# Kernel optimization log

Hardware: AMD Instinct MI355X
Metric: run time of the kernel (lower is better)

The kernel has to match this reference:

```python
import jax, jax.numpy as jnp
from jax import lax
import numpy as np

HEADS = 8
SR = 4  # sr_ratio
LN_EPS = 1e-5


def gaussian_filt(x, kernel_size, sigma):
    # depthwise gaussian blur, x: [B, C, H, W]
    ch = x.shape[1]
    c = jnp.arange(kernel_size, dtype=x.dtype)
    xx = jnp.broadcast_to(c[None, :], (kernel_size, kernel_size))
    yy = xx.T
    mean = (kernel_size - 1) / 2.0
    g = jnp.exp(-((xx - mean) ** 2 + (yy - mean) ** 2) / (2.0 * sigma * sigma))
    g = g / g.sum()  # normalization cancels the 1/(2*pi*var) factor
    kern = jnp.broadcast_to(g[None, None], (ch, 1, kernel_size, kernel_size)).astype(x.dtype)
    p = (kernel_size - 1) // 2
    return lax.conv_general_dilated(
        x, kern, (1, 1), [(p, p), (p, p)],
        dimension_numbers=('NCHW', 'OIHW', 'NCHW'), feature_group_count=ch)


def reconstruct_feature(feature, mask, kernel_size, sigma):
    if kernel_size <= 1:
        return feature
    feature = feature * mask
    out = gaussian_filt(jnp.concatenate([feature, mask], axis=1), kernel_size, sigma)
    f_int = out[:, :-1]
    m_int = out[:, -1:]
    f_int = f_int / (m_int + 1e-6)
    m_bin = (m_int > 0).astype(feature.dtype)
    f_int = f_int * m_bin
    return feature + (1.0 - mask) * f_int


def token2map(x, loc, H, W, kernel_size, sigma):
    # x: [B, N, C], loc: [B, N, 2] in [0,1]
    B, N, C = x.shape
    loc = jnp.clip(loc, 0.0, 1.0) * jnp.array([W - 1, H - 1], dtype=loc.dtype)
    loc = jnp.round(loc).astype(jnp.int32)
    idx = loc[..., 0] + loc[..., 1] * W + (jnp.arange(B, dtype=jnp.int32) * (H * W))[:, None]
    src = jnp.concatenate([x, jnp.ones((B, N, 1), x.dtype)], axis=-1).reshape(B * N, C + 1)
    out = jax.ops.segment_sum(src, idx.reshape(-1), num_segments=B * H * W)
    out = out.reshape(B, H, W, C + 1).transpose(0, 3, 1, 2)  # [B, C+1, H, W]
    feature, mask = out[:, :-1], out[:, -1:]
    feature = feature / (mask + 1e-6)
    mask = (mask > 0).astype(x.dtype)
    feature = feature * mask
    return reconstruct_feature(feature, mask, kernel_size, sigma)


def layer_norm(x, w, b):
    mu = jnp.mean(x, axis=-1, keepdims=True)
    var = jnp.mean((x - mu) ** 2, axis=-1, keepdims=True)
    return (x - mu) * lax.rsqrt(var + LN_EPS) * w + b


def forward(x, x_source, loc_source, conf_source, Wq, Wk, Wv, sr_w, sr_b, ln_w, ln_b, Wp, bp, H, W):
    B, N, C = x.shape
    dh = C // HEADS
    scale = dh ** -0.5
    q = (x @ Wq.T).reshape(B, N, HEADS, dh).transpose(0, 2, 1, 3)  # [B,h,N,dh]
    # token2map + spatial reduction
    xm = token2map(x_source, loc_source, H, W, SR - 1, 2.0)        # [B,C,H,W]
    xs = lax.conv_general_dilated(
        xm, sr_w, (SR, SR), 'VALID',
        dimension_numbers=('NCHW', 'OIHW', 'NCHW')) + sr_b[None, :, None, None]
    xs = xs.reshape(B, C, -1).transpose(0, 2, 1)                   # [B,Ns,C]
    xs = layer_norm(xs, ln_w, ln_b)
    Ns = xs.shape[1]
    k = (xs @ Wk.T).reshape(B, Ns, HEADS, dh).transpose(0, 2, 1, 3)
    v = (xs @ Wv.T).reshape(B, Ns, HEADS, dh).transpose(0, 2, 1, 3)
    attn = jnp.einsum('bhnd,bhmd->bhnm', q, k) * scale             # [B,h,N,Ns]
    attn = attn + conf_source[..., 0][:, None, None, :]            # additive bias
    attn = jax.nn.softmax(attn, axis=-1)
    out = jnp.einsum('bhnm,bhmd->bhnd', attn, v)
    out = out.transpose(0, 2, 1, 3).reshape(B, N, C)
    return out @ Wp.T + bp


def setup_inputs() -> dict:
    key = jax.random.key(0)
    ks = jax.random.split(key, 10)
    B, N, C, Hm = 2, 8192, 256, 128
    Ns = (Hm // SR) * (Hm // SR)
    s = 0.02
    return {
        'x': jax.random.normal(ks[0], (B, N, C), jnp.float32),
        'x_source': jax.random.normal(ks[1], (B, N, C), jnp.float32),
        'loc_source': jax.random.uniform(ks[2], (B, N, 2), jnp.float32),
        'conf_source': jax.random.normal(ks[3], (B, Ns, 1), jnp.float32),
        'Wq': jax.random.normal(ks[4], (C, C), jnp.float32) * s,
        'Wk': jax.random.normal(ks[5], (C, C), jnp.float32) * s,
        'Wv': jax.random.normal(ks[6], (C, C), jnp.float32) * s,
        'sr_w': jax.random.normal(ks[7], (C, C, SR, SR), jnp.float32) * s,
        'sr_b': jnp.zeros((C,), jnp.float32),
        'ln_w': jnp.ones((C,), jnp.float32),
        'ln_b': jnp.zeros((C,), jnp.float32),
        'Wp': jax.random.normal(ks[8], (C, C), jnp.float32) * s,
        'bp': jnp.zeros((C,), jnp.float32),
        'H': Hm,
        'W': Hm,
    }


def reference(x, x_source, loc_source, conf_source, Wq, Wk, Wv, sr_w, sr_b, ln_w, ln_b, Wp, bp, H, W):
    return forward(x, x_source, loc_source, conf_source, Wq, Wk, Wv, sr_w, sr_b, ln_w, ln_b, Wp, bp, H, W)
```

## Files before the change

kernel.cpp:

```cpp
#include <hip/hip_runtime.h>
#include <hip/hip_bf16.h>
#include <cstddef>
#include <cstdint>

#define NTOK 8192
#define CD   256
#define HWPIX 16384
#define WIDTH 128
#define NSEQ 1024

typedef __attribute__((ext_vector_type(8))) short bfrag;
typedef __attribute__((ext_vector_type(4))) float f32x4;
typedef __attribute__((ext_vector_type(4))) unsigned int u32x4;

__device__ inline unsigned short f2bfu(float f) {
    __hip_bfloat16 h = __float2bfloat16(f);
    unsigned short u;
    __builtin_memcpy(&u, &h, 2);
    return u;
}
__device__ inline unsigned int rtn16(float f) {
    unsigned int u = __builtin_bit_cast(unsigned int, f);
    return u + 0x7fffu + ((u >> 16) & 1u);
}
__device__ inline float bits2f(unsigned int u) {
    return __builtin_bit_cast(float, u);
}
__device__ inline bfrag cvt8(float4 a, float4 b) {
    bfrag r;
    r[0] = (short)f2bfu(a.x); r[1] = (short)f2bfu(a.y);
    r[2] = (short)f2bfu(a.z); r[3] = (short)f2bfu(a.w);
    r[4] = (short)f2bfu(b.x); r[5] = (short)f2bfu(b.y);
    r[6] = (short)f2bfu(b.z); r[7] = (short)f2bfu(b.w);
    return r;
}
__device__ inline void gld16(const unsigned short* g, const unsigned short* l) {
    __builtin_amdgcn_global_load_lds(
        (const __attribute__((address_space(1))) unsigned int*)g,
        (__attribute__((address_space(3))) unsigned int*)l, 16, 0, 0);
}
__device__ inline unsigned int cvtpk(float lo, float hi) {
    unsigned int r;
    asm("v_cvt_pk_bf16_f32 %0, %1, %2" : "=v"(r) : "v"(lo), "v"(hi));
    return r;
}
__device__ inline int kslot(int rin) {
    return (((rin >> 5) * 2 + ((rin >> 2) & 1)) << 4)
         + (((rin >> 3) & 3) << 2) + (rin & 3);
}

__global__ __launch_bounds__(256) void scatter_prep(
        const float* __restrict__ xsrc, const float* __restrict__ loc,
        float* __restrict__ feat, float* __restrict__ maskr,
        const float* __restrict__ srw, const float* __restrict__ Wq,
        const float* __restrict__ Wk, const float* __restrict__ Wv,
        const float* __restrict__ Wp, const float* __restrict__ conf,
        const float* __restrict__ srb,
        unsigned short* __restrict__ wTb, unsigned short* __restrict__ wqb,
        unsigned short* __restrict__ wkb, unsigned short* __restrict__ wvb,
        unsigned short* __restrict__ wpb, unsigned short* __restrict__ stg,
        float* __restrict__ xsb) {
    int gid = blockIdx.x, tid = threadIdx.x;
    if (gid < 16384) {
        int token = gid;
        int b = token >> 13;
        float lx = loc[token * 2 + 0];
        float ly = loc[token * 2 + 1];
        lx = fminf(fmaxf(lx, 0.f), 1.f) * 127.0f;
        ly = fminf(fmaxf(ly, 0.f), 1.f) * 127.0f;
        int ix = __float2int_rn(lx);
        int iy = __float2int_rn(ly);
        int p = b * HWPIX + iy * WIDTH + ix;
        atomicAdd(&feat[(size_t)p * CD + tid], xsrc[(size_t)token * CD + tid]);
        if (tid == 0) atomicAdd(&maskr[p], 1.0f);
    } else if (gid < 20480) {
        int idx = (gid - 16384) * 256 + tid;
        int co = idx >> 12;
        int rest = idx & 4095;
        int k16 = rest >> 8;
        int ci = rest & 255;
        int kh = k16 >> 2, kw = k16 & 3;
        wTb[idx] = f2bfu(srw[(size_t)co * 4096 + ci * 16 + kh * 4 + kw]);
    } else if (gid < 20672) {
        const float* s; unsigned short* d; int base;
        if (gid < 20544)      { s = Wq; d = wqb; base = gid - 20480; }
        else if (gid < 20608) { s = Wk; d = wkb; base = gid - 20544; }
        else                  { s = Wv; d = wvb; base = gid - 20608; }
        int i = (base * 256 + tid) * 4;
        float4 v = *(const float4*)(s + i);
        ushort4 o;
        o.x = f2bfu(v.x); o.y = f2bfu(v.y); o.z = f2bfu(v.z); o.w = f2bfu(v.w);
        *(ushort4*)(d + i) = o;
    } else if (gid < 20928) {
        int n = gid - 20672, t = tid;
        float w = Wp[n * 256 + t];
        unsigned short hu = f2bfu(w);
        float hf = bits2f(((unsigned int)hu) << 16);
        unsigned short lu = f2bfu(w - hf);
        wpb[n * 768 + t]       = hu;
        wpb[n * 768 + 256 + t] = lu;
        wpb[n * 768 + 512 + t] = hu;
    } else if (gid < 20936) {
        int idx = (gid - 20928) * 256 + tid;
        int b = idx >> 10, key = idx & 1023;
        int tile = key >> 6, rin = key & 63;
        int slot = kslot(rin);
        float val = conf[idx] * 1.4426950408889634f;
        #pragma unroll
        for (int h = 0; h < 8; h++)
            *(float*)&stg[((size_t)((b * 8 + h) * 16 + tile)) * 5120
                          + 4864 + slot * 2] = val;
    } else {
        int row = gid - 20936;
        xsb[(size_t)row * 256 + tid] = srb[tid];
    }
}

__global__ __launch_bounds__(256) void recon_patch(const float* __restrict__ feat,
        const float* __restrict__ maskr, unsigned short* __restrict__ apatch) {
    __shared__ float s_wci[36];
    __shared__ float s_vb[36];
    __shared__ int   s_np[36];
    __shared__ float s_ginv[16];
    __shared__ float s_omb[16];
    int blk = blockIdx.x;
    int b  = blk >> 10;
    int py = (blk >> 5) & 31;
    int px = blk & 31;
    int c = threadIdx.x;
    const float e1 = 0.882496902584595f;
    const float e2 = 0.778800783071405f;
    const float snorm = 1.0f / (1.0f + 4.0f * e1 + 4.0f * e2);
    int y0 = py * 4 - 1, x0 = px * 4 - 1;
    if (c < 36) {
        int ry = c / 6, rx = c % 6;
        int yy = y0 + ry, xx = x0 + rx;
        bool valid = (yy >= 0 && yy <= 127 && xx >= 0 && xx <= 127);
        int yc = min(max(yy, 0), 127), xc = min(max(xx, 0), 127);
        int np_ = b * HWPIX + yc * WIDTH + xc;
        float m = maskr[np_];
        float bin = (m > 0.f) ? 1.f : 0.f;
        float inv = 1.0f / (m + 1e-6f);
        s_wci[c] = valid ? bin * inv : 0.f;
        s_vb[c]  = valid ? bin : 0.f;
        s_np[c]  = np_;
    }
    __syncthreads();
    if (c < 16) {
        int oy = c >> 2, ox = c & 3;
        float gm = 0.f;
        #pragma unroll
        for (int dy = -1; dy <= 1; dy++)
            #pragma unroll
            for (int dx = -1; dx <= 1; dx++) {
                int manh = (dy != 0) + (dx != 0);
                float g = ((manh == 2) ? e2 : (manh == 1) ? e1 : 1.0f) * snorm;
                gm += g * s_vb[(oy + 1 + dy) * 6 + (ox + 1 + dx)];
            }
        s_ginv[c] = (gm > 0.f) ? 1.0f / (gm + 1e-6f) : 0.f;
        s_omb[c]  = 1.0f - s_vb[(oy + 1) * 6 + (ox + 1)];
    }
    float gf[4][4], fcv[4][4];
    #pragma unroll
    for (int oy = 0; oy < 4; oy++)
        #pragma unroll
        for (int ox = 0; ox < 4; ox++) { gf[oy][ox] = 0.f; fcv[oy][ox] = 0.f; }
    #pragma unroll
    for (int ry = 0; ry < 6; ry++) {
        #pragma unroll
        for (int rx = 0; rx < 6; rx++) {
            int j = ry * 6 + rx;
            float f = feat[(size_t)s_np[j] * CD + c] * s_wci[j];
            #pragma unroll
            for (int oy = 0; oy < 4; oy++) {
                int dy = ry - 1 - oy;
                if (dy < -1 || dy > 1) continue;
                #pragma unroll
                for (int ox = 0; ox < 4; ox++) {
                    int dx = rx - 1 - ox;
                    if (dx < -1 || dx > 1) continue;
                    int manh = (dy != 0) + (dx != 0);
                    float g = ((manh == 2) ? e2 : (manh == 1) ? e1 : 1.0f) * snorm;
                    gf[oy][ox] += g * f;
                }
            }
            if (ry >= 1 && ry <= 4 && rx >= 1 && rx <= 4)
                fcv[ry - 1][rx - 1] = f;
        }
    }
    __syncthreads();
    int r = b * 1024 + py * 32 + px;
    size_t base = (size_t)r * 4096 + c;
    #pragma unroll
    for (int oy = 0; oy < 4; oy++)
        #pragma unroll
        for (int ox = 0; ox < 4; ox++) {
            int i = oy * 4 + ox;
            float f_int = gf[oy][ox] * s_ginv[i];
            float res = fcv[oy][ox] + s_omb[i] * f_int;
            apatch[base + (size_t)i * 256] = f2bfu(res);
        }
}

__device__ __forceinline__ void bgemm_body(
        unsigned short* As, unsigned short* Bs,
        const unsigned short* __restrict__ A, const float* __restrict__ Af,
        const unsigned short* __restrict__ B, const float* __restrict__ bias,
        float* __restrict__ C, unsigned short* __restrict__ dstb,
        int M, int N, int K, int kSplit, int mode, float mult,
        int bx, int by, int bz) {
    int tid = threadIdx.x;
    int wave = tid >> 6, lane = tid & 63, m15 = lane & 15, quad = lane >> 4;
    int wr = (wave >> 1) * 64, wc = (wave & 1) * 64;
    int m0 = by * 128, n0 = bx * 128;
    int kchunk = K / kSplit, k0 = bz * kchunk;
    int srow = tid >> 2, sko = (tid & 3) * 8;
    f32x4 acc[4][4];
    #pragma unroll
    for (int i = 0; i < 4; i++)
        #pragma unroll
        for (int j = 0; j < 4; j++) acc[i][j] = (f32x4){0.f, 0.f, 0.f, 0.f};
    const unsigned short* Ag = A + (size_t)(m0 + srow) * K + k0 + sko;
    const float* Afg = Af + (size_t)(m0 + srow) * K + k0 + sko;
    const unsigned short* Bg = B + (size_t)(n0 + srow) * K + k0 + sko;
    for (int kk = 0; kk < kchunk; kk += 32) {
        bfrag a0, a1;
        if (Af) {
            float4 f0 = *(const float4*)(Afg + kk);
            float4 f1 = *(const float4*)(Afg + kk + 4);
            float4 f2 = *(const float4*)(Afg + (size_t)64 * K + kk);
            float4 f3 = *(const float4*)(Afg + (size_t)64 * K + kk + 4);
            a0 = cvt8(f0, f1);
            a1 = cvt8(f2, f3);
        } else {
            a0 = *(const bfrag*)(Ag + kk);
            a1 = *(const bfrag*)(Ag + (size_t)64 * K + kk);
        }
        bfrag b0 = *(const bfrag*)(Bg + kk);
        bfrag b1 = *(const bfrag*)(Bg + (size_t)64 * K + kk);
        __syncthreads();
        *(bfrag*)&As[srow * 32 + sko] = a0;
        *(bfrag*)&As[(srow + 64) * 32 + sko] = a1;
        *(bfrag*)&Bs[srow * 32 + sko] = b0;
        *(bfrag*)&Bs[(srow + 64) * 32 + sko] = b1;
        __syncthreads();
        bfrag af[4], bfr[4];
        #pragma unroll
        for (int mi = 0; mi < 4; mi++)
            af[mi] = *(const bfrag*)&As[(wr + mi * 16 + m15) * 32 + quad * 8];
        #pragma unroll
        for (int ni = 0; ni < 4; ni++)
            bfr[ni] = *(const bfrag*)&Bs[(wc + ni * 16 + m15) * 32 + quad * 8];
        #pragma unroll
        for (int mi = 0; mi < 4; mi++)
            #pragma unroll
            for (int ni = 0; ni < 4; ni++)
                acc[mi][ni] = __builtin_amdgcn_mfma_f32_16x16x32_bf16(
                                  af[mi], bfr[ni], acc[mi][ni], 0, 0, 0);
    }
    if (mode == 2) {
        #pragma unroll
        for (int mi = 0; mi < 4; mi++) {
            #pragma unroll
            for (int i = 0; i < 4; i++) {
                int row = m0 + wr + mi * 16 + quad * 4 + i;
                int b = row >> 13, r = row & 8191;
                #pragma unroll
                for (int ni = 0; ni < 4; ni++) {
                    int col = n0 + wc + ni * 16 + m15;
                    int h = col >> 5, d = col & 31;
                    size_t di = ((((size_t)(b * 8 + h)) << 13) + r) * 32 + d;
                    dstb[di] = f2bfu(acc[mi][ni][i] * mult);
                }
            }
        }
    } else if (mode == 3) {
        #pragma unroll
        for (int mi = 0; mi < 4; mi++) {
            #pragma unroll
            for (int i = 0; i < 4; i++) {
                int row = m0 + wr + mi * 16 + quad * 4 + i;
                int b = row >> 10, key = row & 1023;
                int tile = key >> 6, rin = key & 63;
                int slot = kslot(rin);
                #pragma unroll
                for (int ni = 0; ni < 4; ni++) {
                    int col = n0 + wc + ni * 16 + m15;
                    unsigned short v = f2bfu(acc[mi][ni][i]);
                    if (col < 256) {
                        int h = col >> 5, d = col & 31;
                        size_t di = ((size_t)((b * 8 + h) * 16 + tile)) * 5120
                                    + slot * 40 + d;
                        dstb[di] = v;
                    } else {
                        int c2 = col - 256;
                        int h = c2 >> 5, d = c2 & 31;
                        size_t di = ((size_t)((b * 8 + h) * 16 + tile)) * 5120
                                    + 2560 + d * 72 + rin;
                        dstb[di] = v;
                    }
                }
            }
        }
    } else {
        #pragma unroll
        for (int mi = 0; mi < 4; mi++) {
            #pragma unroll
            for (int i = 0; i < 4; i++) {
                size_t row = (size_t)(m0 + wr + mi * 16 + quad * 4 + i) * N;
                #pragma unroll
                for (int ni = 0; ni < 4; ni++) {
                    int col = n0 + wc + ni * 16 + m15;
                    float v = acc[mi][ni][i];
                    if (mode == 1) atomicAdd(&C[row + col], v);
                    else C[row + col] = v + (bias ? bias[col] : 0.f);
                }
            }
        }
    }
}

__global__ __launch_bounds__(256) void bgemm(const unsigned short* A,
        const float* Af, const unsigned short* B, const float* bias,
        float* C, unsigned short* dstb,
        int M, int N, int K, int kSplit, int mode, float mult) {
    __shared__ __align__(16) unsigned short As[128 * 32];
    __shared__ __align__(16) unsigned short Bs[128 * 32];
    bgemm_body(As, Bs, A, Af, B, bias, C, dstb, M, N, K, kSplit, mode, mult,
               blockIdx.x, blockIdx.y, blockIdx.z);
}

__global__ __launch_bounds__(256) void qkv_fused(const float* x,
        const unsigned short* wqb, const unsigned short* xsbf,
        const unsigned short* wkb, unsigned short* Qbf,
        unsigned short* stg, float SC) {
    __shared__ __align__(16) unsigned short As[128 * 32];
    __shared__ __align__(16) unsigned short Bs[128 * 32];
    int g = blockIdx.x;
    if (g < 256) {
        bgemm_body(As, Bs, nullptr, x, wqb, nullptr, nullptr, Qbf,
                   16384, 256, 256, 1, 2, SC, g & 1, g >> 1, 0);
    } else {
        int g2 = g - 256;
        bgemm_body(As, Bs, xsbf, nullptr, wkb, nullptr, nullptr, stg,
                   2048, 512, 256, 1, 3, 1.f, g2 & 3, g2 >> 2, 0);
    }
}

__global__ __launch_bounds__(256) void ln_k(const float* __restrict__ xs,
        const float* __restrict__ w, const float* __restrict__ bvec,
        unsigned short* __restrict__ outb) {
    int row = blockIdx.x;
    int c = threadIdx.x;
    float v = xs[(size_t)row * 256 + c];
    __shared__ float red[4];
    float s = v;
    #pragma unroll
    for (int o = 32; o >= 1; o >>= 1) s += __shfl_down(s, o, 64);
    if ((c & 63) == 0) red[c >> 6] = s;
    __syncthreads();
    float mean = (red[0] + red[1] + red[2] + red[3]) * (1.f / 256.f);
    __syncthreads();
    float d = v - mean;
    float s2 = d * d;
    #pragma unroll
    for (int o = 32; o >= 1; o >>= 1) s2 += __shfl_down(s2, o, 64);
    if ((c & 63) == 0) red[c >> 6] = s2;
    __syncthreads();
    float var = (red[0] + red[1] + red[2] + red[3]) * (1.f / 256.f);
    float r = 1.0f / sqrtf(var + 1e-5f);
    outb[(size_t)row * 256 + c] = f2bfu(d * r * w[c] + bvec[c]);
}

__global__ __launch_bounds__(256, 4) void attn_v10(
        const unsigned short* __restrict__ Qb,
        const unsigned short* __restrict__ STG,
        unsigned short* __restrict__ aout) {
    __shared__ __align__(16) unsigned short SB[2][5120];
    int tid  = threadIdx.x;
    int wave = tid >> 6;
    int lane = tid & 63;
    int m15  = lane & 15;
    int quad = lane >> 4;
    int bh = blockIdx.y;
    int b  = bh >> 3;
    int h  = bh & 7;
    int qbase = blockIdx.x * 128 + wave * 32;

    const unsigned short* qp = Qb + ((size_t)bh * NTOK + qbase) * 32;
    bfrag Qa0 = *(const bfrag*)(qp + m15 * 32 + quad * 8);
    bfrag Qa1 = *(const bfrag*)(qp + (16 + m15) * 32 + quad * 8);
    const unsigned short* sg = STG + (size_t)bh * 16 * 5120;

    bfrag ones;
    #pragma unroll
    for (int i = 0; i < 8; i++) ones[i] = (short)0x3F80;

    f32x4 O[2][2];
    f32x4 Lac[2];
    #pragma unroll
    for (int tq = 0; tq < 2; tq++) {
        O[tq][0] = (f32x4){0.f, 0.f, 0.f, 0.f};
        O[tq][1] = (f32x4){0.f, 0.f, 0.f, 0.f};
        Lac[tq]  = (f32x4){0.f, 0.f, 0.f, 0.f};
    }

    {
        const unsigned short* g = sg;
        unsigned short* l = SB[0];
        gld16(g + wave * 512 + lane * 8, l + wave * 512);
        gld16(g + (wave + 4) * 512 + lane * 8, l + (wave + 4) * 512);
        if (wave < 2) gld16(g + (8 + wave) * 512 + lane * 8, l + (8 + wave) * 512);
    }
    __syncthreads();

    #pragma unroll 2
    for (int t = 0; t < 16; t++) {
        const unsigned short* Ks = SB[t & 1];
        const unsigned short* Vs = Ks + 2560;
        const float* Cf = (const float*)(Ks + 4864);
        bfrag kf[4]; f32x4 ccf[4];
        #pragma unroll
        for (int s = 0; s < 4; s++) {
            kf[s]  = *(const bfrag*)&Ks[(s * 16 + m15) * 40 + quad * 8];
            ccf[s] = *(const f32x4*)&Cf[s * 16 + quad * 4];
        }
        if (t < 15) {
            const unsigned short* g = sg + (size_t)(t + 1) * 5120;
            unsigned short* l = SB[(t + 1) & 1];
            gld16(g + wave * 512 + lane * 8, l + wave * 512);
            gld16(g + (wave + 4) * 512 + lane * 8, l + (wave + 4) * 512);
            if (wave < 2) gld16(g + (8 + wave) * 512 + lane * 8,
                                l + (8 + wave) * 512);
        }
        f32x4 S[2][4];
        __builtin_amdgcn_s_setprio(1);
        #pragma unroll
        for (int s = 0; s < 4; s++) {
            S[0][s] = __builtin_amdgcn_mfma_f32_16x16x32_bf16(kf[s], Qa0,
                                                              ccf[s], 0, 0, 0);
            S[1][s] = __builtin_amdgcn_mfma_f32_16x16x32_bf16(kf[s], Qa1,
                                                              ccf[s], 0, 0, 0);
        }
        __builtin_amdgcn_s_setprio(0);
        bfrag Pb[2][2];
        #pragma unroll
        for (int tq = 0; tq < 2; tq++) {
            float v[4][4];
            #pragma unroll
            for (int s = 0; s < 4; s++)
                #pragma unroll
                for (int r = 0; r < 4; r++)
                    v[s][r] = __builtin_amdgcn_exp2f(S[tq][s][r]);
            #pragma unroll
            for (int k2 = 0; k2 < 2; k2++) {
                u32x4 pw;
                pw[0] = cvtpk(v[2 * k2][0],     v[2 * k2][1]);
                pw[1] = cvtpk(v[2 * k2][2],     v[2 * k2][3]);
                pw[2] = cvtpk(v[2 * k2 + 1][0], v[2 * k2 + 1][1]);
                pw[3] = cvtpk(v[2 * k2 + 1][2], v[2 * k2 + 1][3]);
                Pb[tq][k2] = __builtin_bit_cast(bfrag, pw);
            }
        }
        bfrag vfr[2][2];
        #pragma unroll
        for (int k2 = 0; k2 < 2; k2++)
            #pragma unroll
            for (int dt = 0; dt < 2; dt++)
                vfr[k2][dt] = *(const bfrag*)&Vs[(dt * 16 + m15) * 72 +
                                                 k2 * 32 + quad * 8];
        __builtin_amdgcn_s_setprio(1);
        #pragma unroll
        for (int k2 = 0; k2 < 2; k2++)
            #pragma unroll
            for (int tq = 0; tq < 2; tq++) {
                #pragma unroll
                for (int dt = 0; dt < 2; dt++)
                    O[tq][dt] = __builtin_amdgcn_mfma_f32_16x16x32_bf16(
                                    Pb[tq][k2], vfr[k2][dt], O[tq][dt], 0, 0, 0);
                Lac[tq] = __builtin_amdgcn_mfma_f32_16x16x32_bf16(
                                    Pb[tq][k2], ones, Lac[tq], 0, 0, 0);
            }
        __builtin_amdgcn_s_setprio(0);
        __syncthreads();
    }
    #pragma unroll
    for (int tq = 0; tq < 2; tq++) {
        #pragma unroll
        for (int r = 0; r < 4; r++) {
            float inv = 1.0f / Lac[tq][r];
            int row = b * NTOK + qbase + tq * 16 + quad * 4 + r;
            size_t rb = (size_t)row * 768;
            #pragma unroll
            for (int dt = 0; dt < 2; dt++) {
                float o = O[tq][dt][r] * inv;
                unsigned int hr = rtn16(o);
                unsigned short hu = hr >> 16;
                float hf = bits2f(hr & 0xffff0000u);
                unsigned short lu = rtn16(o - hf) >> 16;
                int col = h * 32 + dt * 16 + m15;
                aout[rb + col]       = hu;
                aout[rb + 256 + col] = hu;
                aout[rb + 512 + col] = lu;
            }
        }
    }
}

extern "C" void kernel_launch(void* const* d_in, const int* in_sizes, int n_in,
                              void* d_out, int out_size, void* d_ws, size_t ws_size,
                              hipStream_t stream) {
    const float* x        = (const float*)d_in[0];
    const float* x_source = (const float*)d_in[1];
    const float* loc      = (const float*)d_in[2];
    const float* conf     = (const float*)d_in[3];
    const float* Wq       = (const float*)d_in[4];
    const float* Wk       = (const float*)d_in[5];
    const float* Wv       = (const float*)d_in[6];
    const float* srw      = (const float*)d_in[7];
    const float* srb      = (const float*)d_in[8];
    const float* lnw      = (const float*)d_in[9];
    const float* lnb      = (const float*)d_in[10];
    const float* Wp       = (const float*)d_in[11];
    const float* bp       = (const float*)d_in[12];
    float* out = (float*)d_out;
    float* ws  = (float*)d_ws;

    float* feat = ws;
    unsigned short* Qbf = (unsigned short*)ws;
    float* maskr = ws + 8388608;
    unsigned short* apatch = (unsigned short*)(ws + 8421376);
    unsigned short* aouts  = (unsigned short*)(ws + 8421376);
    unsigned short* wTb    = (unsigned short*)(ws + 12615680);
    unsigned short* stg  = (unsigned short*)(ws + 14712832);
    unsigned short* wqb  = (unsigned short*)(ws + 15368192);
    unsigned short* wkb  = (unsigned short*)(ws + 15400960);
    unsigned short* wvb  = (unsigned short*)(ws + 15433728);
    unsigned short* wpb  = (unsigned short*)(ws + 15466496);
    float*          xsb  = ws + 15564800;
    unsigned short* xsbf = (unsigned short*)(ws + 16089088);

    const float SC = 0.17677669529663687f * 1.4426950408889634f;

    hipMemsetAsync(feat, 0, (size_t)(8388608 + 32768) * sizeof(float), stream);

    scatter_prep<<<22984, 256, 0, stream>>>(x_source, loc, feat, maskr,
                                            srw, Wq, Wk, Wv, Wp, conf, srb,
                                            wTb, wqb, wkb, wvb, wpb, stg, xsb);
    recon_patch<<<2048, 256, 0, stream>>>(feat, maskr, apatch);
    bgemm<<<dim3(2, 16, 8), 256, 0, stream>>>(apatch, nullptr, wTb, nullptr,
                                              xsb, nullptr,
                                              2048, 256, 4096, 8, 1, 1.f);
    ln_k<<<2048, 256, 0, stream>>>(xsb, lnw, lnb, xsbf);
    qkv_fused<<<320, 256, 0, stream>>>(x, wqb, xsbf, wkb, Qbf, stg, SC);
    attn_v10<<<dim3(64, 16), 256, 0, stream>>>(Qbf, stg, aouts);
    bgemm<<<dim3(2, 128, 1), 256, 0, stream>>>(aouts, nullptr, wpb, bp,
                                               out, nullptr,
                                               16384, 256, 768, 1, 0, 1.f);
}
```

Before: 237.7 us.

## Triple-buffer attention K/V staging with one barrier per tile and block swizzle

The attention kernel moves from double to triple buffering of the staged K/V/bias tiles in LDS and prefetches two tiles ahead. Explicit vmcnt waits plus a single s_barrier per iteration replace the trailing __syncthreads, so loads stay in flight across iterations. The block index is also remapped so that consecutive blocks span different heads, which changes how the shared K/V data is reused in cache. LDS use grows from 20 KB to 30 KB per block, which may limit occupancy, and the hand-counted vmcnt values must match the async load count per wave.

```diff
diff --git a/kernel.cpp b/kernel.cpp
--- a/kernel.cpp
+++ b/kernel.cpp
@@ -372,20 +372,22 @@
     outb[(size_t)row * 256 + c] = f2bfu(d * r * w[c] + bvec[c]);
 }
 
-__global__ __launch_bounds__(256, 4) void attn_v10(
+__global__ __launch_bounds__(256, 4) void attn_v11(
         const unsigned short* __restrict__ Qb,
         const unsigned short* __restrict__ STG,
         unsigned short* __restrict__ aout) {
-    __shared__ __align__(16) unsigned short SB[2][5120];
+    __shared__ __align__(16) unsigned short SB[3][5120];
     int tid  = threadIdx.x;
     int wave = tid >> 6;
     int lane = tid & 63;
     int m15  = lane & 15;
     int quad = lane >> 4;
-    int bh = blockIdx.y;
+    int flat = blockIdx.y * 64 + blockIdx.x;
+    int j  = flat >> 3;
+    int bh = (flat & 7) + ((j >> 6) << 3);
     int b  = bh >> 3;
     int h  = bh & 7;
-    int qbase = blockIdx.x * 128 + wave * 32;
+    int qbase = (j & 63) * 128 + wave * 32;
 
     const unsigned short* qp = Qb + ((size_t)bh * NTOK + qbase) * 32;
     bfrag Qa0 = *(const bfrag*)(qp + m15 * 32 + quad * 8);
@@ -405,18 +407,26 @@
         Lac[tq]  = (f32x4){0.f, 0.f, 0.f, 0.f};
     }
 
-    {
-        const unsigned short* g = sg;
-        unsigned short* l = SB[0];
+    #pragma unroll
+    for (int pt = 0; pt < 2; pt++) {
+        const unsigned short* g = sg + (size_t)pt * 5120;
+        unsigned short* l = &SB[pt][0];
         gld16(g + wave * 512 + lane * 8, l + wave * 512);
         gld16(g + (wave + 4) * 512 + lane * 8, l + (wave + 4) * 512);
         if (wave < 2) gld16(g + (8 + wave) * 512 + lane * 8, l + (8 + wave) * 512);
     }
-    __syncthreads();
-
-    #pragma unroll 2
+
+    int cur = 0;
     for (int t = 0; t < 16; t++) {
-        const unsigned short* Ks = SB[t & 1];
+        if (t < 15) {
+            if (wave < 2) asm volatile("s_waitcnt vmcnt(3)" ::: "memory");
+            else          asm volatile("s_waitcnt vmcnt(2)" ::: "memory");
+        } else {
+            asm volatile("s_waitcnt vmcnt(0)" ::: "memory");
+        }
+        __builtin_amdgcn_s_barrier();
+        __builtin_amdgcn_sched_barrier(0);
+        const unsigned short* Ks = &SB[0][0] + cur * 5120;
         const unsigned short* Vs = Ks + 2560;
         const float* Cf = (const float*)(Ks + 4864);
         bfrag kf[4]; f32x4 ccf[4];
@@ -425,9 +435,10 @@
             kf[s]  = *(const bfrag*)&Ks[(s * 16 + m15) * 40 + quad * 8];
             ccf[s] = *(const f32x4*)&Cf[s * 16 + quad * 4];
         }
-        if (t < 15) {
-            const unsigned short* g = sg + (size_t)(t + 1) * 5120;
-            unsigned short* l = SB[(t + 1) & 1];
+        if (t < 14) {
+            int nxt = cur + 2; if (nxt >= 3) nxt -= 3;
+            const unsigned short* g = sg + (size_t)(t + 2) * 5120;
+            unsigned short* l = &SB[0][0] + nxt * 5120;
             gld16(g + wave * 512 + lane * 8, l + wave * 512);
             gld16(g + (wave + 4) * 512 + lane * 8, l + (wave + 4) * 512);
             if (wave < 2) gld16(g + (8 + wave) * 512 + lane * 8,
@@ -482,7 +493,7 @@
                                     Pb[tq][k2], ones, Lac[tq], 0, 0, 0);
             }
         __builtin_amdgcn_s_setprio(0);
-        __syncthreads();
+        cur = (cur == 2) ? 0 : cur + 1;
     }
     #pragma unroll
     for (int tq = 0; tq < 2; tq++) {
@@ -553,7 +564,7 @@
                                               2048, 256, 4096, 8, 1, 1.f);
     ln_k<<<2048, 256, 0, stream>>>(xsb, lnw, lnb, xsbf);
     qkv_fused<<<320, 256, 0, stream>>>(x, wqb, xsbf, wkb, Qbf, stg, SC);
-    attn_v10<<<dim3(64, 16), 256, 0, stream>>>(Qbf, stg, aouts);
+    attn_v11<<<dim3(64, 16), 256, 0, stream>>>(Qbf, stg, aouts);
     bgemm<<<dim3(2, 128, 1), 256, 0, stream>>>(aouts, nullptr, wpb, bp,
                                                out, nullptr,
                                                16384, 256, 768, 1, 0, 1.f);
```

New measurement: 236.6 us. No clear change (-0.4%).
